# Kernel tuning notes

Hardware: AMD Instinct MI355X
Metric: run time of the kernel (lower is better)

Reference implementation:

```python
import jax, jax.numpy as jnp
import numpy as np

# pywt Wavelet('db4') decomposition filters (8 taps)
DB4_DEC_LO = np.array([-0.010597401784997278, 0.032883011666982945,
                       0.030841381835986965, -0.18703481171888114,
                       -0.027983769416983849, 0.63088076792959036,
                       0.71484657055254153, 0.23037781330885523], dtype=np.float32)
# quadrature mirror: dec_hi[k] = (-1)^(k+1) * dec_lo[F-1-k]
DB4_DEC_HI = (DB4_DEC_LO[::-1] * np.array([-1.0, 1.0] * 4, dtype=np.float32)).astype(np.float32)
LEVELS = 4


def _dwt_step(x, lo, hi):
    """One pywt.dwt level, mode='symmetric'. x: [B, L] -> (cA, cD) each [B, floor((L+F-1)/2)]."""
    F = lo.shape[0]
    # symmetric half-sample extension by F-1 on each side, then drop one sample so a
    # stride-2 VALID correlation picks the odd-indexed outputs of the full valid conv
    ext = jnp.pad(x, ((0, 0), (F - 1, F - 1)), mode='symmetric')[:, 1:]
    inp = ext[:, None, :]                                # [B, 1, Lext]
    # pywt convolves (flipped filter); lax conv is correlation, so flip filters here
    ker = jnp.stack([lo[::-1], hi[::-1]])[:, None, :]    # [2, 1, F]
    y = jax.lax.conv_general_dilated(inp, ker, window_strides=(2,), padding='VALID',
                                     dimension_numbers=('NCH', 'OIH', 'NCH'))
    return y[:, 0, :], y[:, 1, :]


def _wavedec(x, levels):
    lo = jnp.asarray(DB4_DEC_LO)
    hi = jnp.asarray(DB4_DEC_HI)
    details = []
    ca = x
    for _ in range(levels):
        ca, cd = _dwt_step(ca, lo, hi)
        details.append(cd)
    # pywt ordering: [cA_n, cD_n, cD_{n-1}, ..., cD_1]
    return [ca] + details[::-1]


def setup_inputs() -> dict:
    key = jax.random.key(0)
    kx, kw, kb = jax.random.split(key, 3)
    B, L = 4096, 4096
    x = jax.random.normal(kx, (B, L), dtype=jnp.float32)
    weights = jax.random.normal(kw, (LEVELS + 1, 1), dtype=jnp.float32)
    bias = jax.random.normal(kb, (LEVELS + 1, 1), dtype=jnp.float32)
    return {"x": x, "weights": weights, "bias": bias}


def reference(x, weights, bias):
    coeffs = _wavedec(x, LEVELS)
    # per-band learnable affine: coeff_j * w_j + b_j (w_j, b_j scalars broadcast over [B, L_j])
    out = tuple(c * weights[j, 0] + bias[j, 0] for j, c in enumerate(coeffs))
    return out
```

## Files before the change

### kernel.cpp

```cpp
#include <hip/hip_runtime.h>

#define NT 256

#define L0 -0.010597401784997278f
#define L1f 0.032883011666982945f
#define L2f 0.030841381835986965f
#define L3f -0.18703481171888114f
#define L4f -0.02798376941698385f
#define L5f 0.6308807679295904f
#define L6f 0.7148465705525415f
#define L7f 0.23037781330885523f


constexpr int B_ROWS = 4096;
constexpr int LVL1 = 4096, N1 = 2051, N2 = 1029, N3 = 518, N4 = 262;
constexpr size_t OFF_CA4 = 0;
constexpr size_t OFF_CD4 = (size_t)B_ROWS * N4;
constexpr size_t OFF_CD3 = OFF_CD4 + (size_t)B_ROWS * N4;
constexpr size_t OFF_CD2 = OFF_CD3 + (size_t)B_ROWS * N3;
constexpr size_t OFF_CD1 = OFF_CD2 + (size_t)B_ROWS * N2;

__device__ __forceinline__ void lds_barrier() {
    asm volatile("s_waitcnt lgkmcnt(0)" ::: "memory");
    __builtin_amdgcn_s_barrier();
    asm volatile("" ::: "memory");
}

__device__ __forceinline__ void dwt_one_clamped(const float* __restrict__ src, int L, int t,
                                                float& slo, float& shi) {
    constexpr float LOR[8] = {L7f, L6f, L5f, L4f, L3f, L2f, L1f, L0};
    constexpr float HIR[8] = {L0, -L1f, L2f, -L3f, L4f, -L5f, L6f, -L7f};
    const int idx0 = 2 * t - 6;
    slo = 0.f; shi = 0.f;
#pragma unroll
    for (int m = 0; m < 8; ++m) {
        int q = idx0 + m;
        q = (q < 0) ? (-1 - q) : q;
        q = (q >= L) ? (2 * L - 1 - q) : q;
        const float v = src[q];
        slo = fmaf(LOR[m], v, slo);
        shi = fmaf(HIR[m], v, shi);
    }
}

template <bool SCALE_A>
__device__ __forceinline__ void dwt_level_blk(const float* __restrict__ src, int L,
                                              float* __restrict__ dstA, float wa, float ba,
                                              float* __restrict__ outD, float wd, float bd) {
    constexpr float LOR[8] = {L7f, L6f, L5f, L4f, L3f, L2f, L1f, L0};
    constexpr float HIR[8] = {L0, -L1f, L2f, -L3f, L4f, -L5f, L6f, -L7f};
    const int N = (L + 7) >> 1;
    const int Mmax = (L - 8) >> 3;
    const int tid = threadIdx.x;

    const float h0 = wd * HIR[0], h1 = wd * HIR[1], h2 = wd * HIR[2], h3 = wd * HIR[3],
                h4 = wd * HIR[4], h5 = wd * HIR[5], h6 = wd * HIR[6], h7 = wd * HIR[7];
    const float g0 = wa * LOR[0], g1 = wa * LOR[1], g2 = wa * LOR[2], g3 = wa * LOR[3],
                g4 = wa * LOR[4], g5 = wa * LOR[5], g6 = wa * LOR[6], g7 = wa * LOR[7];

    for (int m = 1 + tid; m <= Mmax; m += NT) {
        const float4* p = reinterpret_cast<const float4*>(src) + (2 * m - 2);
        const float4 v0 = p[0], v1 = p[1], v2 = p[2], v3 = p[3];
        const float W[16] = {v0.x, v0.y, v0.z, v0.w, v1.x, v1.y, v1.z, v1.w,
                             v2.x, v2.y, v2.z, v2.w, v3.x, v3.y, v3.z, v3.w};
        float accA[4], accD[4];
#pragma unroll
        for (int o = 0; o < 4; ++o) {
            float sd = bd;
            sd = fmaf(h0, W[2 * o + 2], sd);
            sd = fmaf(h1, W[2 * o + 3], sd);
            sd = fmaf(h2, W[2 * o + 4], sd);
            sd = fmaf(h3, W[2 * o + 5], sd);
            sd = fmaf(h4, W[2 * o + 6], sd);
            sd = fmaf(h5, W[2 * o + 7], sd);
            sd = fmaf(h6, W[2 * o + 8], sd);
            sd = fmaf(h7, W[2 * o + 9], sd);
            accD[o] = sd;
            float sa;
            if (SCALE_A) {
                sa = ba;
                sa = fmaf(g0, W[2 * o + 2], sa);
                sa = fmaf(g1, W[2 * o + 3], sa);
                sa = fmaf(g2, W[2 * o + 4], sa);
                sa = fmaf(g3, W[2 * o + 5], sa);
                sa = fmaf(g4, W[2 * o + 6], sa);
                sa = fmaf(g5, W[2 * o + 7], sa);
                sa = fmaf(g6, W[2 * o + 8], sa);
                sa = fmaf(g7, W[2 * o + 9], sa);
            } else {
                sa = LOR[0] * W[2 * o + 2];
                sa = fmaf(LOR[1], W[2 * o + 3], sa);
                sa = fmaf(LOR[2], W[2 * o + 4], sa);
                sa = fmaf(LOR[3], W[2 * o + 5], sa);
                sa = fmaf(LOR[4], W[2 * o + 6], sa);
                sa = fmaf(LOR[5], W[2 * o + 7], sa);
                sa = fmaf(LOR[6], W[2 * o + 8], sa);
                sa = fmaf(LOR[7], W[2 * o + 9], sa);
            }
            accA[o] = sa;
        }
        const int t0 = 4 * m;
        if (SCALE_A) {
            dstA[t0 + 0] = accA[0]; dstA[t0 + 1] = accA[1];
            dstA[t0 + 2] = accA[2]; dstA[t0 + 3] = accA[3];
        } else {
            float4 qa; qa.x = accA[0]; qa.y = accA[1]; qa.z = accA[2]; qa.w = accA[3];
            *(reinterpret_cast<float4*>(dstA) + m) = qa;
        }
        outD[t0 + 0] = accD[0]; outD[t0 + 1] = accD[1];
        outD[t0 + 2] = accD[2]; outD[t0 + 3] = accD[3];
    }

    const int NS = N - 4 * Mmax;
    if (tid < NS) {
        const int t = (tid < 4) ? tid : (4 * Mmax + tid);
        float slo, shi;
        dwt_one_clamped(src, L, t, slo, shi);
        dstA[t] = SCALE_A ? fmaf(wa, slo, ba) : slo;
        outD[t] = fmaf(wd, shi, bd);
    }
}

__global__ __launch_bounds__(NT) void lwt_kernel(const float* __restrict__ x,
                                                 const float* __restrict__ w,
                                                 const float* __restrict__ bias,
                                                 float* __restrict__ out) {
    __shared__ __align__(16) float P[N1];
    __shared__ __align__(16) float Q[N2];
    constexpr float LOR[8] = {L7f, L6f, L5f, L4f, L3f, L2f, L1f, L0};
    constexpr float HIR[8] = {L0, -L1f, L2f, -L3f, L4f, -L5f, L6f, -L7f};
    const int row = blockIdx.x;
    const int tid = threadIdx.x;
    const float* __restrict__ xr = x + (size_t)row * LVL1;

    const float w0 = w[0], w1 = w[1], w2 = w[2], w3 = w[3], w4 = w[4];
    const float b0 = bias[0], b1 = bias[1], b2 = bias[2], b3 = bias[3], b4 = bias[4];

    float* outCD1 = out + OFF_CD1 + (size_t)row * N1;
    const float h0 = w4 * HIR[0], h1 = w4 * HIR[1], h2 = w4 * HIR[2], h3 = w4 * HIR[3],
                h4 = w4 * HIR[4], h5 = w4 * HIR[5], h6 = w4 * HIR[6], h7 = w4 * HIR[7];

    for (int m = 1 + tid; m <= 511; m += NT) {
        const float4* p = reinterpret_cast<const float4*>(xr) + (2 * m - 2);
        const float4 v0 = p[0], v1 = p[1], v2 = p[2], v3 = p[3];
        const float W[16] = {v0.x, v0.y, v0.z, v0.w, v1.x, v1.y, v1.z, v1.w,
                             v2.x, v2.y, v2.z, v2.w, v3.x, v3.y, v3.z, v3.w};
        float accA[4], accD[4];
#pragma unroll
        for (int o = 0; o < 4; ++o) {
            float sd = b4;
            sd = fmaf(h0, W[2 * o + 2], sd);
            sd = fmaf(h1, W[2 * o + 3], sd);
            sd = fmaf(h2, W[2 * o + 4], sd);
            sd = fmaf(h3, W[2 * o + 5], sd);
            sd = fmaf(h4, W[2 * o + 6], sd);
            sd = fmaf(h5, W[2 * o + 7], sd);
            sd = fmaf(h6, W[2 * o + 8], sd);
            sd = fmaf(h7, W[2 * o + 9], sd);
            accD[o] = sd;
            float sa = LOR[0] * W[2 * o + 2];
            sa = fmaf(LOR[1], W[2 * o + 3], sa);
            sa = fmaf(LOR[2], W[2 * o + 4], sa);
            sa = fmaf(LOR[3], W[2 * o + 5], sa);
            sa = fmaf(LOR[4], W[2 * o + 6], sa);
            sa = fmaf(LOR[5], W[2 * o + 7], sa);
            sa = fmaf(LOR[6], W[2 * o + 8], sa);
            sa = fmaf(LOR[7], W[2 * o + 9], sa);
            accA[o] = sa;
        }
        const int t0 = 4 * m;
        float4 qa; qa.x = accA[0]; qa.y = accA[1]; qa.z = accA[2]; qa.w = accA[3];
        *(reinterpret_cast<float4*>(P) + m) = qa;
        outCD1[t0 + 0] = accD[0]; outCD1[t0 + 1] = accD[1];
        outCD1[t0 + 2] = accD[2]; outCD1[t0 + 3] = accD[3];
    }
    if (tid < 7) {
        const int t = (tid < 4) ? tid : (2044 + tid);
        float slo, shi;
        dwt_one_clamped(xr, LVL1, t, slo, shi);
        P[t] = slo;
        outCD1[t] = fmaf(w4, shi, b4);
    }

    lds_barrier();
    dwt_level_blk<false>(P, N1, Q, 0.f, 0.f, out + OFF_CD2 + (size_t)row * N2, w3, b3);
    lds_barrier();
    dwt_level_blk<false>(Q, N2, P, 0.f, 0.f, out + OFF_CD3 + (size_t)row * N3, w2, b2);
    lds_barrier();
    dwt_level_blk<true>(P, N3, out + OFF_CA4 + (size_t)row * N4, w0, b0,
                        out + OFF_CD4 + (size_t)row * N4, w1, b1);
}

extern "C" void kernel_launch(void* const* d_in, const int* in_sizes, int n_in,
                              void* d_out, int out_size, void* d_ws, size_t ws_size,
                              hipStream_t stream) {
    const float* x = (const float*)d_in[0];
    const float* wp = (const float*)d_in[1];
    const float* bp = (const float*)d_in[2];
    float* out = (float*)d_out;
    lwt_kernel<<<dim3(B_ROWS), dim3(NT), 0, stream>>>(x, wp, bp, out);
}
```

Before: 27.71 us.

## Pipeline level-1 of the next row with levels 2-4 of the current row

Each block now handles four rows with 512 threads split into two warp-specialized halves. One half computes level-1 DWT of the next row from global memory into a double-buffered LDS array. The other half runs levels 2-4 of the previous row from LDS, staged across three barrier-separated phases. The aim is to hide the serial, low-parallelism deeper levels behind the memory-bound level-1 work. In exchange there are 4x fewer blocks, more LDS per block, and uneven work per phase.

```diff
diff --git a/kernel.cpp b/kernel.cpp
--- a/kernel.cpp
+++ b/kernel.cpp
@@ -1,6 +1,7 @@
 #include <hip/hip_runtime.h>
 
-#define NT 256
+#define NT 512
+#define R_PB 4
 
 #define L0 -0.010597401784997278f
 #define L1f 0.032883011666982945f
@@ -19,6 +20,7 @@
 constexpr size_t OFF_CD3 = OFF_CD4 + (size_t)B_ROWS * N4;
 constexpr size_t OFF_CD2 = OFF_CD3 + (size_t)B_ROWS * N3;
 constexpr size_t OFF_CD1 = OFF_CD2 + (size_t)B_ROWS * N2;
+constexpr int PSTR = 2052;
 
 __device__ __forceinline__ void lds_barrier() {
     asm volatile("s_waitcnt lgkmcnt(0)" ::: "memory");
@@ -44,21 +46,21 @@
 }
 
 template <bool SCALE_A>
-__device__ __forceinline__ void dwt_level_blk(const float* __restrict__ src, int L,
-                                              float* __restrict__ dstA, float wa, float ba,
-                                              float* __restrict__ outD, float wd, float bd) {
+__device__ __forceinline__ void dwt_level_c(const float* __restrict__ src, int L,
+                                            float* __restrict__ dstA, float wa, float ba,
+                                            float* __restrict__ outD, float wd, float bd,
+                                            int tid) {
     constexpr float LOR[8] = {L7f, L6f, L5f, L4f, L3f, L2f, L1f, L0};
     constexpr float HIR[8] = {L0, -L1f, L2f, -L3f, L4f, -L5f, L6f, -L7f};
     const int N = (L + 7) >> 1;
     const int Mmax = (L - 8) >> 3;
-    const int tid = threadIdx.x;
 
     const float h0 = wd * HIR[0], h1 = wd * HIR[1], h2 = wd * HIR[2], h3 = wd * HIR[3],
                 h4 = wd * HIR[4], h5 = wd * HIR[5], h6 = wd * HIR[6], h7 = wd * HIR[7];
     const float g0 = wa * LOR[0], g1 = wa * LOR[1], g2 = wa * LOR[2], g3 = wa * LOR[3],
                 g4 = wa * LOR[4], g5 = wa * LOR[5], g6 = wa * LOR[6], g7 = wa * LOR[7];
 
-    for (int m = 1 + tid; m <= Mmax; m += NT) {
+    for (int m = 1 + tid; m <= Mmax; m += 256) {
         const float4* p = reinterpret_cast<const float4*>(src) + (2 * m - 2);
         const float4 v0 = p[0], v1 = p[1], v2 = p[2], v3 = p[3];
         const float W[16] = {v0.x, v0.y, v0.z, v0.w, v1.x, v1.y, v1.z, v1.w,
@@ -121,74 +123,117 @@
     }
 }
 
-__global__ __launch_bounds__(NT) void lwt_kernel(const float* __restrict__ x,
-                                                 const float* __restrict__ w,
-                                                 const float* __restrict__ bias,
-                                                 float* __restrict__ out) {
-    __shared__ __align__(16) float P[N1];
-    __shared__ __align__(16) float Q[N2];
+__device__ __forceinline__ void l1_do(const float* __restrict__ xr,
+                                      float* __restrict__ Pn,
+                                      float* __restrict__ cd1,
+                                      int m, float w4, float b4) {
     constexpr float LOR[8] = {L7f, L6f, L5f, L4f, L3f, L2f, L1f, L0};
     constexpr float HIR[8] = {L0, -L1f, L2f, -L3f, L4f, -L5f, L6f, -L7f};
-    const int row = blockIdx.x;
+    const float4* p = reinterpret_cast<const float4*>(xr) + (2 * m - 2);
+    const float4 v0 = p[0], v1 = p[1], v2 = p[2], v3 = p[3];
+    const float W[16] = {v0.x, v0.y, v0.z, v0.w, v1.x, v1.y, v1.z, v1.w,
+                         v2.x, v2.y, v2.z, v2.w, v3.x, v3.y, v3.z, v3.w};
+    const float h0 = w4 * HIR[0], h1 = w4 * HIR[1], h2 = w4 * HIR[2], h3 = w4 * HIR[3],
+                h4 = w4 * HIR[4], h5 = w4 * HIR[5], h6 = w4 * HIR[6], h7 = w4 * HIR[7];
+    float accA[4], accD[4];
+#pragma unroll
+    for (int o = 0; o < 4; ++o) {
+        float sd = b4;
+        sd = fmaf(h0, W[2 * o + 2], sd);
+        sd = fmaf(h1, W[2 * o + 3], sd);
+        sd = fmaf(h2, W[2 * o + 4], sd);
+        sd = fmaf(h3, W[2 * o + 5], sd);
+        sd = fmaf(h4, W[2 * o + 6], sd);
+        sd = fmaf(h5, W[2 * o + 7], sd);
+        sd = fmaf(h6, W[2 * o + 8], sd);
+        sd = fmaf(h7, W[2 * o + 9], sd);
+        accD[o] = sd;
+        float sa = LOR[0] * W[2 * o + 2];
+        sa = fmaf(LOR[1], W[2 * o + 3], sa);
+        sa = fmaf(LOR[2], W[2 * o + 4], sa);
+        sa = fmaf(LOR[3], W[2 * o + 5], sa);
+        sa = fmaf(LOR[4], W[2 * o + 6], sa);
+        sa = fmaf(LOR[5], W[2 * o + 7], sa);
+        sa = fmaf(LOR[6], W[2 * o + 8], sa);
+        sa = fmaf(LOR[7], W[2 * o + 9], sa);
+        accA[o] = sa;
+    }
+    const int t0 = 4 * m;
+    float4 qa; qa.x = accA[0]; qa.y = accA[1]; qa.z = accA[2]; qa.w = accA[3];
+    *(reinterpret_cast<float4*>(Pn) + m) = qa;
+    cd1[t0 + 0] = accD[0]; cd1[t0 + 1] = accD[1];
+    cd1[t0 + 2] = accD[2]; cd1[t0 + 3] = accD[3];
+}
+
+__device__ __forceinline__ void l1_specials(const float* __restrict__ xr,
+                                            float* __restrict__ Pn,
+                                            float* __restrict__ cd1,
+                                            int tid, float w4, float b4) {
+    const int t = (tid < 4) ? tid : (2044 + tid);
+    float slo, shi;
+    dwt_one_clamped(xr, LVL1, t, slo, shi);
+    Pn[t] = slo;
+    cd1[t] = fmaf(w4, shi, b4);
+}
+
+__global__ __launch_bounds__(NT) void lwt_pc_kernel(const float* __restrict__ x,
+                                                    const float* __restrict__ w,
+                                                    const float* __restrict__ bias,
+                                                    float* __restrict__ out) {
+    __shared__ __align__(16) float P[2][PSTR];
+    __shared__ __align__(16) float Q[1032];
+    __shared__ __align__(16) float Rb[520];
     const int tid = threadIdx.x;
-    const float* __restrict__ xr = x + (size_t)row * LVL1;
+    const int row0 = blockIdx.x * R_PB;
 
     const float w0 = w[0], w1 = w[1], w2 = w[2], w3 = w[3], w4 = w[4];
     const float b0 = bias[0], b1 = bias[1], b2 = bias[2], b3 = bias[3], b4 = bias[4];
 
-    float* outCD1 = out + OFF_CD1 + (size_t)row * N1;
-    const float h0 = w4 * HIR[0], h1 = w4 * HIR[1], h2 = w4 * HIR[2], h3 = w4 * HIR[3],
-                h4 = w4 * HIR[4], h5 = w4 * HIR[5], h6 = w4 * HIR[6], h7 = w4 * HIR[7];
-
-    for (int m = 1 + tid; m <= 511; m += NT) {
-        const float4* p = reinterpret_cast<const float4*>(xr) + (2 * m - 2);
-        const float4 v0 = p[0], v1 = p[1], v2 = p[2], v3 = p[3];
-        const float W[16] = {v0.x, v0.y, v0.z, v0.w, v1.x, v1.y, v1.z, v1.w,
-                             v2.x, v2.y, v2.z, v2.w, v3.x, v3.y, v3.z, v3.w};
-        float accA[4], accD[4];
-#pragma unroll
-        for (int o = 0; o < 4; ++o) {
-            float sd = b4;
-            sd = fmaf(h0, W[2 * o + 2], sd);
-            sd = fmaf(h1, W[2 * o + 3], sd);
-            sd = fmaf(h2, W[2 * o + 4], sd);
-            sd = fmaf(h3, W[2 * o + 5], sd);
-            sd = fmaf(h4, W[2 * o + 6], sd);
-            sd = fmaf(h5, W[2 * o + 7], sd);
-            sd = fmaf(h6, W[2 * o + 8], sd);
-            sd = fmaf(h7, W[2 * o + 9], sd);
-            accD[o] = sd;
-            float sa = LOR[0] * W[2 * o + 2];
-            sa = fmaf(LOR[1], W[2 * o + 3], sa);
-            sa = fmaf(LOR[2], W[2 * o + 4], sa);
-            sa = fmaf(LOR[3], W[2 * o + 5], sa);
-            sa = fmaf(LOR[4], W[2 * o + 6], sa);
-            sa = fmaf(LOR[5], W[2 * o + 7], sa);
-            sa = fmaf(LOR[6], W[2 * o + 8], sa);
-            sa = fmaf(LOR[7], W[2 * o + 9], sa);
-            accA[o] = sa;
-        }
-        const int t0 = 4 * m;
-        float4 qa; qa.x = accA[0]; qa.y = accA[1]; qa.z = accA[2]; qa.w = accA[3];
-        *(reinterpret_cast<float4*>(P) + m) = qa;
-        outCD1[t0 + 0] = accD[0]; outCD1[t0 + 1] = accD[1];
-        outCD1[t0 + 2] = accD[2]; outCD1[t0 + 3] = accD[3];
-    }
-    if (tid < 7) {
-        const int t = (tid < 4) ? tid : (2044 + tid);
-        float slo, shi;
-        dwt_one_clamped(xr, LVL1, t, slo, shi);
-        P[t] = slo;
-        outCD1[t] = fmaf(w4, shi, b4);
-    }
-
+    {
+        const float* xr = x + (size_t)row0 * LVL1;
+        float* cd1 = out + OFF_CD1 + (size_t)row0 * N1;
+        const int m = 1 + tid;
+        if (m <= 511) l1_do(xr, P[0], cd1, m, w4, b4);
+        if (tid < 7) l1_specials(xr, P[0], cd1, tid, w4, b4);
+    }
     lds_barrier();
-    dwt_level_blk<false>(P, N1, Q, 0.f, 0.f, out + OFF_CD2 + (size_t)row * N2, w3, b3);
-    lds_barrier();
-    dwt_level_blk<false>(Q, N2, P, 0.f, 0.f, out + OFF_CD3 + (size_t)row * N3, w2, b2);
-    lds_barrier();
-    dwt_level_blk<true>(P, N3, out + OFF_CA4 + (size_t)row * N4, w0, b0,
-                        out + OFF_CD4 + (size_t)row * N4, w1, b1);
+
+    for (int i = 1; i <= R_PB; ++i) {
+        const bool doL1 = (i < R_PB);
+        const int rowC = row0 + i - 1;
+        float* Pn = P[i & 1];
+        float* Pc = P[(i - 1) & 1];
+        const float* xr = x + (size_t)(row0 + i) * LVL1;
+        float* cd1 = out + OFF_CD1 + (size_t)(row0 + i) * N1;
+
+        if (tid < 256) {
+            if (doL1 && tid < 128) l1_do(xr, Pn, cd1, 1 + tid, w4, b4);
+        } else {
+            dwt_level_c<false>(Pc, N1, Q, 0.f, 0.f,
+                               out + OFF_CD2 + (size_t)rowC * N2, w3, b3, tid - 256);
+        }
+        lds_barrier();
+
+        if (tid < 256) {
+            if (doL1 && tid < 192) l1_do(xr, Pn, cd1, 129 + tid, w4, b4);
+        } else {
+            dwt_level_c<false>(Q, N2, Rb, 0.f, 0.f,
+                               out + OFF_CD3 + (size_t)rowC * N3, w2, b2, tid - 256);
+        }
+        lds_barrier();
+
+        if (tid < 256) {
+            if (doL1) {
+                if (tid < 191) l1_do(xr, Pn, cd1, 321 + tid, w4, b4);
+                if (tid < 7) l1_specials(xr, Pn, cd1, tid, w4, b4);
+            }
+        } else {
+            dwt_level_c<true>(Rb, N3,
+                              out + OFF_CA4 + (size_t)rowC * N4, w0, b0,
+                              out + OFF_CD4 + (size_t)rowC * N4, w1, b1, tid - 256);
+        }
+        lds_barrier();
+    }
 }
 
 extern "C" void kernel_launch(void* const* d_in, const int* in_sizes, int n_in,
@@ -198,5 +243,5 @@
     const float* wp = (const float*)d_in[1];
     const float* bp = (const float*)d_in[2];
     float* out = (float*)d_out;
-    lwt_kernel<<<dim3(B_ROWS), dim3(NT), 0, stream>>>(x, wp, bp, out);
-}
+    lwt_pc_kernel<<<dim3(B_ROWS / R_PB), dim3(NT), 0, stream>>>(x, wp, bp, out);
+}
```

After: 43.49 us. +56.9%, slower.
